# Kernel optimization log

Hardware: AMD Instinct MI355X
Metric: run time of the kernel (lower is better)

Reference implementation:

```python
import jax, jax.numpy as jnp
import numpy as np

NUM_LEVELS = 4
N = 524288


def _e8_roots() -> np.ndarray:
    """The 240 roots of the E8 lattice, float32 [240, 8].

    Type 1 (112): all permutations of (+-1, +-1, 0^6).
    Type 2 (128): (+-1/2)^8 with an even number of minus signs.
    """
    roots = []
    for i in range(8):
        for j in range(i + 1, 8):
            for si in (1.0, -1.0):
                for sj in (1.0, -1.0):
                    v = np.zeros(8, dtype=np.float64)
                    v[i] = si
                    v[j] = sj
                    roots.append(v)
    for m in range(256):
        signs = np.array([1.0 if ((m >> k) & 1) == 0 else -1.0 for k in range(8)])
        if int((signs < 0).sum()) % 2 == 0:
            roots.append(0.5 * signs)
    out = np.stack(roots).astype(np.float32)
    assert out.shape == (240, 8)
    return out


def setup_inputs() -> dict:
    key = jax.random.key(0)
    x = jax.random.normal(key, (N, 8), dtype=jnp.float32)
    roots = jnp.asarray(_e8_roots())  # [240, 8] fixed codebook (buffer)
    return {"x": x, "roots": roots}


def reference(x, roots):
    # Residual multi-level nearest-neighbor quantization against E8 roots.
    x_flat = x.reshape(-1, 8)                       # [N, 8]
    r2 = jnp.sum(roots * roots, axis=1)[None, :]    # [1, 240]
    qsum = jnp.zeros_like(x_flat)
    residual = x_flat
    indices = []
    for _level in range(NUM_LEVELS):
        res2 = jnp.sum(residual * residual, axis=1, keepdims=True)      # [N, 1]
        # squared euclidean distances, clamped at 0 for numerical safety
        d2 = jnp.clip(res2 + r2 - 2.0 * (residual @ roots.T), 0.0)      # [N, 240]
        idx = jnp.argmin(d2, axis=-1)                                   # [N]
        qsum = qsum + roots[idx]                                        # gather
        residual = x_flat - qsum
        indices.append(idx)
    quantized = qsum.reshape(x.shape)
    # straight-through estimator: value == quantized, grad flows via x
    quantized_ste = quantized + x - jax.lax.stop_gradient(x)
    qerr = jnp.mean(
        (jax.lax.stop_gradient(x) - jax.lax.stop_gradient(quantized)) ** 2
    )
    idx_stack = jnp.stack(indices).reshape((NUM_LEVELS,) + x.shape[:-1])
    return quantized_ste, idx_stack, qerr
```

## Files before the change

kernel.cpp:

```cpp
#include <hip/hip_runtime.h>
#include <math.h>


__global__ __launch_bounds__(256) void e8_quant_kernel(
    const float* __restrict__ x, const float* __restrict__ roots,
    float* __restrict__ out, float* __restrict__ partials, int nrow) {
#pragma clang fp contract(off)
  __shared__ float lroots[240 * 8];
  __shared__ float wred[4];
  for (int t = threadIdx.x; t < 240 * 8; t += 256) lroots[t] = roots[t];
  __syncthreads();

  const int row = blockIdx.x * 256 + threadIdx.x;
  const bool active = row < nrow;
  float e = 0.f;

  if (active) {
    const float4 xa = *(const float4*)(x + (size_t)row * 8);
    const float4 xb = *(const float4*)(x + (size_t)row * 8 + 4);
    float xr[8] = {xa.x, xa.y, xa.z, xa.w, xb.x, xb.y, xb.z, xb.w};
    float qs[8] = {0.f, 0.f, 0.f, 0.f, 0.f, 0.f, 0.f, 0.f};
    float r[8];
#pragma unroll
    for (int k = 0; k < 8; ++k) r[k] = xr[k];

    float* out_idx = out + (size_t)nrow * 8;

#pragma unroll 1
    for (int lvl = 0; lvl < 4; ++lvl) {
      const float q0 = r[0] * r[0], q1 = r[1] * r[1], q2 = r[2] * r[2],
                  q3 = r[3] * r[3], q4 = r[4] * r[4], q5 = r[5] * r[5],
                  q6 = r[6] * r[6], q7 = r[7] * r[7];
      const float res2 = ((q0 + q1) + (q2 + q3)) + ((q4 + q5) + (q6 + q7));
      const float s = res2 + 2.0f;

      const unsigned u0 = __float_as_uint(r[0]), u1 = __float_as_uint(r[1]),
                     u2 = __float_as_uint(r[2]), u3 = __float_as_uint(r[3]),
                     u4 = __float_as_uint(r[4]), u5 = __float_as_uint(r[5]),
                     u6 = __float_as_uint(r[6]), u7 = __float_as_uint(r[7]);
      const float m0v = __uint_as_float(u0 & 0x7fffffffu),
                  m1v = __uint_as_float(u1 & 0x7fffffffu),
                  m2v = __uint_as_float(u2 & 0x7fffffffu),
                  m3v = __uint_as_float(u3 & 0x7fffffffu),
                  m4v = __uint_as_float(u4 & 0x7fffffffu),
                  m5v = __uint_as_float(u5 & 0x7fffffffu),
                  m6v = __uint_as_float(u6 & 0x7fffffffu),
                  m7v = __uint_as_float(u7 & 0x7fffffffu);
      const int sb0 = (int)(u0 >> 31), sb1 = (int)(u1 >> 31),
                sb2 = (int)(u2 >> 31), sb3 = (int)(u3 >> 31),
                sb4 = (int)(u4 >> 31), sb5 = (int)(u5 >> 31),
                sb6 = (int)(u6 >> 31), sb7 = (int)(u7 >> 31);
      const int msk = sb0 | (sb1 << 1) | (sb2 << 2) | (sb3 << 3) |
                      (sb4 << 4) | (sb5 << 5) | (sb6 << 6) | (sb7 << 7);
      const int par = __popc(msk) & 1;
      const float Sabs =
          ((m0v + m1v) + (m2v + m3v)) + ((m4v + m5v) + (m6v + m7v));

      const int K0 = 0 | (sb0 << 3), K1 = 1 | (sb1 << 3), K2 = 2 | (sb2 << 3),
                K3 = 3 | (sb3 << 3), K4 = 4 | (sb4 << 3), K5 = 5 | (sb5 << 3),
                K6 = 6 | (sb6 << 3), K7 = 7 | (sb7 << 3);

      const bool g01 = m1v > m0v;
      const float h01 = fmaxf(m0v, m1v), l01 = fminf(m0v, m1v);
      const int hk01 = g01 ? K1 : K0, lk01 = g01 ? K0 : K1;
      const bool g23 = m3v > m2v;
      const float h23 = fmaxf(m2v, m3v), l23 = fminf(m2v, m3v);
      const int hk23 = g23 ? K3 : K2, lk23 = g23 ? K2 : K3;
      const bool g45 = m5v > m4v;
      const float h45 = fmaxf(m4v, m5v), l45 = fminf(m4v, m5v);
      const int hk45 = g45 ? K5 : K4, lk45 = g45 ? K4 : K5;
      const bool g67 = m7v > m6v;
      const float h67 = fmaxf(m6v, m7v), l67 = fminf(m6v, m7v);
      const int hk67 = g67 ? K7 : K6, lk67 = g67 ? K6 : K7;
      const bool qg0 = h23 > h01;
      const float qh0 = fmaxf(h01, h23);
      const int qhk0 = qg0 ? hk23 : hk01;
      const float sA0 = qg0 ? l23 : l01;
      const int sAk0 = qg0 ? lk23 : lk01;
      const float sB0 = qg0 ? h01 : h23;
      const int sBk0 = qg0 ? hk01 : hk23;
      const float loL0 = qg0 ? l01 : l23;
      const bool qx0 = sB0 > sA0;
      const float qs0v = fmaxf(sA0, sB0);
      const int qsk0 = qx0 ? sBk0 : sAk0;
      const float qt0 = qx0 ? fmaxf(sA0, loL0) : sB0;
      const bool qg1 = h67 > h45;
      const float qh1 = fmaxf(h45, h67);
      const int qhk1 = qg1 ? hk67 : hk45;
      const float sA1 = qg1 ? l67 : l45;
      const int sAk1 = qg1 ? lk67 : lk45;
      const float sB1 = qg1 ? h45 : h67;
      const int sBk1 = qg1 ? hk45 : hk67;
      const float loL1 = qg1 ? l45 : l67;
      const bool qx1 = sB1 > sA1;
      const float qs1v = fmaxf(sA1, sB1);
      const int qsk1 = qx1 ? sBk1 : sAk1;
      const float qt1 = qx1 ? fmaxf(sA1, loL1) : sB1;
      const bool fg = qh1 > qh0;
      const float A1v = fmaxf(qh0, qh1);
      const int A1K = fg ? qhk1 : qhk0;
      const float fA = fg ? qs1v : qs0v;
      const int fAk = fg ? qsk1 : qsk0;
      const float fB = fg ? qh0 : qh1;
      const int fBk = fg ? qhk0 : qhk1;
      const float tW = fg ? qt1 : qt0;
      const float sL = fg ? qs0v : qs1v;
      const bool fh = fB > fA;
      const float A2v = fmaxf(fA, fB);
      const int A2K = fh ? fBk : fAk;
      const float A3v = fh ? fmaxf(fA, sL) : fmaxf(tW, fB);

      const bool n0 = l23 < l01;
      const float mn0 = fminf(l01, l23);
      const int mnk0 = n0 ? lk23 : lk01;
      const float pr0 = n0 ? h23 : h01;
      const float ot0 = fmaxf(l01, l23);
      const bool n1 = l67 < l45;
      const float mn1 = fminf(l45, l67);
      const int mnk1 = n1 ? lk67 : lk45;
      const float pr1 = n1 ? h67 : h45;
      const float ot1 = fmaxf(l45, l67);
      const bool nf = mn1 < mn0;
      const float Aminv = fminf(mn0, mn1);
      const int AminK = nf ? mnk1 : mnk0;
      const float prW = nf ? pr1 : pr0;
      const float otW = nf ? ot1 : ot0;
      const float mnL = fmaxf(mn0, mn1);
      const float Amin2v = fminf(prW, fminf(otW, mnL));

      const float dT1 = A1v + A2v;
      const float halfS = 0.5f * Sabs;
      const float dT2 = par ? (halfS - Aminv) : halfS;

      const int p1 = A1K & 7, p2 = A2K & 7;
      const int s1b = A1K >> 3, s2b = A2K >> 3;
      const bool o12 = p1 < p2;
      const int imn = o12 ? p1 : p2, jmx = o12 ? p2 : p1;
      const int sIb = o12 ? s1b : s2b, sJb = o12 ? s2b : s1b;
      const int pbase = imn * 7 - ((imn * (imn - 1)) >> 1) + (jmx - imn - 1);
      const int t1idx = (pbase << 2) | (sIb << 1) | sJb;

      const int mp = AminK & 7;
      const int mf = par ? (msk ^ (1 << mp)) : msk;
      const int t2idx = 112 + (mf >> 1);

      const bool useT1 = dT1 > dT2;
      const float thr =
          (res2 + 2.0f * Sabs + 2.0f) * 7.6293945e-06f;
      const bool okc = fabsf(dT1 - dT2) > thr;
      const bool okt = useT1 ? ((A2v - A3v) > thr)
                             : (par ? ((Amin2v - Aminv) > thr)
                                    : ((Aminv + Amin2v) > thr));
      const int ok = okc && okt;

      int bi = useT1 ? t1idx : t2idx;

      if (__any(!ok)) {
        float best = 3.4028235e38f;
        int be = 0;
        int ci = 0;
#pragma unroll
        for (int i = 0; i < 8; ++i) {
#pragma unroll
          for (int j = i + 1; j < 8; ++j) {
            const float a = r[i] + r[j];
            const float b = r[i] - r[j];
            float d;
            d = fmaf(-2.f, a, s);
            if (d < best) { best = d; be = ci + 0; }
            d = fmaf(-2.f, b, s);
            if (d < best) { best = d; be = ci + 1; }
            d = fmaf(2.f, b, s);
            if (d < best) { best = d; be = ci + 2; }
            d = fmaf(2.f, a, s);
            if (d < best) { best = d; be = ci + 3; }
            ci += 4;
          }
        }
        const float h0 = 0.5f * r[0], h1 = 0.5f * r[1], h2 = 0.5f * r[2],
                    h3 = 0.5f * r[3], h4 = 0.5f * r[4], h5 = 0.5f * r[5],
                    h6 = 0.5f * r[6], h7 = 0.5f * r[7];
        for (int t = 0; t < 128; ++t) {
          const int m = (t << 1) | (__popc(t) & 1);
          float v = (m & 1) ? -h0 : h0;
          v = (m & 2) ? (v - h1) : (v + h1);
          v = (m & 4) ? (v - h2) : (v + h2);
          v = (m & 8) ? (v - h3) : (v + h3);
          v = (m & 16) ? (v - h4) : (v + h4);
          v = (m & 32) ? (v - h5) : (v + h5);
          v = (m & 64) ? (v - h6) : (v + h6);
          v = (m & 128) ? (v - h7) : (v + h7);
          const float d = fmaf(-2.f, v, s);
          if (d < best) { best = d; be = 112 + t; }
        }
        bi = be;
      }

      out_idx[(size_t)lvl * nrow + row] = (float)bi;

      const float4 ra = *(const float4*)(lroots + bi * 8);
      const float4 rb = *(const float4*)(lroots + bi * 8 + 4);
      qs[0] += ra.x; qs[1] += ra.y; qs[2] += ra.z; qs[3] += ra.w;
      qs[4] += rb.x; qs[5] += rb.y; qs[6] += rb.z; qs[7] += rb.w;
#pragma unroll
      for (int k = 0; k < 8; ++k) r[k] = xr[k] - qs[k];
    }

    float o[8];
#pragma unroll
    for (int k = 0; k < 8; ++k) o[k] = (qs[k] + xr[k]) - xr[k];
    *(float4*)(out + (size_t)row * 8) = make_float4(o[0], o[1], o[2], o[3]);
    *(float4*)(out + (size_t)row * 8 + 4) = make_float4(o[4], o[5], o[6], o[7]);

#pragma unroll
    for (int k = 0; k < 8; ++k) e = fmaf(r[k], r[k], e);
  }

#pragma unroll
  for (int off = 32; off > 0; off >>= 1) e += __shfl_down(e, off, 64);
  const int lane = threadIdx.x & 63, wv = threadIdx.x >> 6;
  if (lane == 0) wred[wv] = e;
  __syncthreads();
  if (threadIdx.x == 0)
    partials[blockIdx.x] = (wred[0] + wred[1]) + (wred[2] + wred[3]);
}

__global__ __launch_bounds__(256) void qerr_reduce_kernel(
    const float* __restrict__ partials, float* __restrict__ out, int n,
    size_t pos, float scale) {
#pragma clang fp contract(off)
  __shared__ float wred[4];
  float e = 0.f;
  for (int i = threadIdx.x; i < n; i += 256) e += partials[i];
#pragma unroll
  for (int off = 32; off > 0; off >>= 1) e += __shfl_down(e, off, 64);
  const int lane = threadIdx.x & 63, wv = threadIdx.x >> 6;
  if (lane == 0) wred[wv] = e;
  __syncthreads();
  if (threadIdx.x == 0)
    out[pos] = ((wred[0] + wred[1]) + (wred[2] + wred[3])) * scale;
}

extern "C" void kernel_launch(void* const* d_in, const int* in_sizes, int n_in,
                              void* d_out, int out_size, void* d_ws,
                              size_t ws_size, hipStream_t stream) {
  const float* x = (const float*)d_in[0];
  const float* roots = (const float*)d_in[1];
  float* out = (float*)d_out;
  float* partials = (float*)d_ws;

  const int nrow = in_sizes[0] / 8;
  const int nblocks = (nrow + 255) / 256;

  e8_quant_kernel<<<nblocks, 256, 0, stream>>>(x, roots, out, partials, nrow);

  const size_t qerr_pos = (size_t)nrow * 12;
  const float scale = 1.0f / (float)((size_t)nrow * 8);
  qerr_reduce_kernel<<<1, 256, 0, stream>>>(partials, out, nblocks, qerr_pos,
                                            scale);
}
```

Measured before the change: 110.3 us.

## Split E8 fallback into per-type exhaustive searches with targeted re-evaluation

Splits the uncertain-case fallback into two independent searches: the 112 type-1 roots are scanned only when the type-1 winner margin is ambiguous, and the 128 type-2 roots only when the type-2 winner is ambiguous. When only the cross-type comparison is close, it recomputes just the chosen type-2 candidate's distance exactly and picks between the two. The threshold constant is also tightened, so fewer rows take the fallback. This cuts how often and how much brute-force work the wavefront does, at the cost of more divergent branches and some numerical tie-breaking risk.

```diff
diff --git a/kernel.cpp b/kernel.cpp
--- a/kernel.cpp
+++ b/kernel.cpp
@@ -128,7 +128,7 @@
       const float mnL = fmaxf(mn0, mn1);
       const float Amin2v = fminf(prW, fminf(otW, mnL));
 
-      const float dT1 = A1v + A2v;
+      const float dT1r = A1v + A2v;
       const float halfS = 0.5f * Sabs;
       const float dT2 = par ? (halfS - Aminv) : halfS;
 
@@ -144,57 +144,100 @@
       const int mf = par ? (msk ^ (1 << mp)) : msk;
       const int t2idx = 112 + (mf >> 1);
 
-      const bool useT1 = dT1 > dT2;
       const float thr =
-          (res2 + 2.0f * Sabs + 2.0f) * 7.6293945e-06f;
-      const bool okc = fabsf(dT1 - dT2) > thr;
-      const bool okt = useT1 ? ((A2v - A3v) > thr)
-                             : (par ? ((Amin2v - Aminv) > thr)
-                                    : ((Aminv + Amin2v) > thr));
-      const int ok = okc && okt;
-
-      int bi = useT1 ? t1idx : t2idx;
-
-      if (__any(!ok)) {
-        float best = 3.4028235e38f;
-        int be = 0;
-        int ci = 0;
-#pragma unroll
-        for (int i = 0; i < 8; ++i) {
-#pragma unroll
-          for (int j = i + 1; j < 8; ++j) {
-            const float a = r[i] + r[j];
-            const float b = r[i] - r[j];
-            float d;
-            d = fmaf(-2.f, a, s);
-            if (d < best) { best = d; be = ci + 0; }
-            d = fmaf(-2.f, b, s);
-            if (d < best) { best = d; be = ci + 1; }
-            d = fmaf(2.f, b, s);
-            if (d < best) { best = d; be = ci + 2; }
-            d = fmaf(2.f, a, s);
-            if (d < best) { best = d; be = ci + 3; }
-            ci += 4;
+          (res2 + 2.0f * Sabs + 2.0f) * 1.9073486e-06f;
+      const bool a1 = (A2v - A3v) > thr;
+      const bool a2 = par ? ((Amin2v - Aminv) > thr)
+                          : ((Aminv + Amin2v) > thr);
+      const bool c = fabsf(dT1r - dT2) > thr;
+
+      float d1 = fmaf(-2.f, dT1r, s);
+      int i1 = t1idx;
+      float d2x = 0.f;
+      int i2 = t2idx;
+
+      if (__any(!a1)) {
+        if (!a1) {
+          float best = 3.4028235e38f;
+          int be = 0;
+          int ci = 0;
+#pragma unroll
+          for (int i = 0; i < 8; ++i) {
+#pragma unroll
+            for (int j = i + 1; j < 8; ++j) {
+              const float a = r[i] + r[j];
+              const float b = r[i] - r[j];
+              float d;
+              d = fmaf(-2.f, a, s);
+              if (d < best) { best = d; be = ci + 0; }
+              d = fmaf(-2.f, b, s);
+              if (d < best) { best = d; be = ci + 1; }
+              d = fmaf(2.f, b, s);
+              if (d < best) { best = d; be = ci + 2; }
+              d = fmaf(2.f, a, s);
+              if (d < best) { best = d; be = ci + 3; }
+              ci += 4;
+            }
           }
+          d1 = best;
+          i1 = be;
         }
-        const float h0 = 0.5f * r[0], h1 = 0.5f * r[1], h2 = 0.5f * r[2],
-                    h3 = 0.5f * r[3], h4 = 0.5f * r[4], h5 = 0.5f * r[5],
-                    h6 = 0.5f * r[6], h7 = 0.5f * r[7];
-        for (int t = 0; t < 128; ++t) {
-          const int m = (t << 1) | (__popc(t) & 1);
-          float v = (m & 1) ? -h0 : h0;
-          v = (m & 2) ? (v - h1) : (v + h1);
-          v = (m & 4) ? (v - h2) : (v + h2);
-          v = (m & 8) ? (v - h3) : (v + h3);
-          v = (m & 16) ? (v - h4) : (v + h4);
-          v = (m & 32) ? (v - h5) : (v + h5);
-          v = (m & 64) ? (v - h6) : (v + h6);
-          v = (m & 128) ? (v - h7) : (v + h7);
-          const float d = fmaf(-2.f, v, s);
-          if (d < best) { best = d; be = 112 + t; }
+      }
+
+      if (__any(!a2)) {
+        if (!a2) {
+          const float h0 = 0.5f * r[0], h1 = 0.5f * r[1], h2 = 0.5f * r[2],
+                      h3 = 0.5f * r[3], h4 = 0.5f * r[4], h5 = 0.5f * r[5],
+                      h6 = 0.5f * r[6], h7 = 0.5f * r[7];
+          float best2 = 3.4028235e38f;
+          int bt = 0;
+#pragma unroll
+          for (int t = 0; t < 128; ++t) {
+            const int m = (t << 1) | (__popc(t) & 1);
+            float v = (m & 1) ? -h0 : h0;
+            v = (m & 2) ? (v - h1) : (v + h1);
+            v = (m & 4) ? (v - h2) : (v + h2);
+            v = (m & 8) ? (v - h3) : (v + h3);
+            v = (m & 16) ? (v - h4) : (v + h4);
+            v = (m & 32) ? (v - h5) : (v + h5);
+            v = (m & 64) ? (v - h6) : (v + h6);
+            v = (m & 128) ? (v - h7) : (v + h7);
+            const float d = fmaf(-2.f, v, s);
+            if (d < best2) { best2 = d; bt = t; }
+          }
+          d2x = best2;
+          i2 = 112 + bt;
         }
-        bi = be;
       }
+
+      if (__any(!c && a2)) {
+        if (!c && a2) {
+          const int flip = par ? mp : 8;
+          float t0 = 0.5f * m0v, t1v = 0.5f * m1v, t2v = 0.5f * m2v,
+                t3v = 0.5f * m3v, t4v = 0.5f * m4v, t5v = 0.5f * m5v,
+                t6v = 0.5f * m6v, t7v = 0.5f * m7v;
+          t0 = (flip == 0) ? -t0 : t0;
+          t1v = (flip == 1) ? -t1v : t1v;
+          t2v = (flip == 2) ? -t2v : t2v;
+          t3v = (flip == 3) ? -t3v : t3v;
+          t4v = (flip == 4) ? -t4v : t4v;
+          t5v = (flip == 5) ? -t5v : t5v;
+          t6v = (flip == 6) ? -t6v : t6v;
+          t7v = (flip == 7) ? -t7v : t7v;
+          float v = t0;
+          v = v + t1v;
+          v = v + t2v;
+          v = v + t3v;
+          v = v + t4v;
+          v = v + t5v;
+          v = v + t6v;
+          v = v + t7v;
+          d2x = fmaf(-2.f, v, s);
+        }
+      }
+
+      const int bi = c ? ((dT1r > dT2) ? i1 : i2)
+                       : ((d1 <= d2x) ? i1 : i2);
 
       out_idx[(size_t)lvl * nrow + row] = (float)bi;
 
```

Result: faster. 92.89 us (-15.8%).
